# Performance work log

Hardware: AMD Instinct MI355X
Metric: run time of the kernel (lower is better)

Reference implementation:

```python
import jax, jax.numpy as jnp
import numpy as np

NEG = -1e30  # finite stand-in for -inf; exp underflows to 0 in fp32, grads stay finite


def setup_inputs() -> dict:
    key = jax.random.key(0)
    k1, k2, k3 = jax.random.split(key, 3)
    B, N, M = 64, 1024, 1024
    m = jax.random.normal(k1, (B, N, M), dtype=jnp.float32)
    nrows = jax.random.randint(k2, (B,), 0, N, dtype=jnp.int64) if jax.config.read('jax_enable_x64') else jax.random.randint(k2, (B,), 0, N, dtype=jnp.int32)
    ncols = jax.random.randint(k3, (B,), 0, M, dtype=jnp.int32)
    nrows = nrows.astype(jnp.int32)
    return {"m": m, "nrows": nrows, "ncols": ncols}


def reference(m, nrows, ncols):
    max_iter, tau = 20, 1.0
    B, N, M = m.shape  # N <= M -> no-transpose branch of the original
    row_valid = jnp.arange(N)[None, :, None] < nrows[:, None, None]  # [B,N,1]
    col_valid = jnp.arange(M)[None, None, :] < ncols[:, None, None]  # [B,1,M]
    valid = row_valid & col_valid                                    # [B,N,M]

    log_m = jnp.where(valid, m / tau, NEG)

    def step(lm, _):
        # even iteration: normalize rows (sum over columns)
        lse_r = jax.scipy.special.logsumexp(lm, axis=2, keepdims=True)  # [B,N,1]
        lm = jnp.where(valid, lm - lse_r, NEG)
        # odd iteration: normalize columns (sum over rows)
        lse_c = jax.scipy.special.logsumexp(lm, axis=1, keepdims=True)  # [B,1,M]
        lm = jnp.where(valid, lm - lse_c, NEG)
        return lm, None

    log_m, _ = jax.lax.scan(step, log_m, None, length=max_iter // 2)
    return jnp.where(valid, jnp.exp(log_m), 0.0)
```

## Files before the change

kernel.cpp:

```cpp
#include <hip/hip_runtime.h>
#include <math.h>


#define BIGNEG (-1e30f)
#define LOG2E 1.44269504f
typedef _Float16 h16;
struct alignas(16) h8 { h16 h[8]; };
typedef float f4 __attribute__((ext_vector_type(4)));

#define NN 1024
#define MM 1024
#define NBLK 16

__device__ __forceinline__ float wave_sum64(float v) {
#pragma unroll
    for (int o = 32; o > 0; o >>= 1) v += __shfl_xor(v, o, 64);
    return v;
}

__device__ __forceinline__ float ld_coh(const float* p) {
    return __hip_atomic_load(p, __ATOMIC_RELAXED, __HIP_MEMORY_SCOPE_AGENT);
}
__device__ __forceinline__ void st_coh(float* p, float v) {
    __hip_atomic_store(p, v, __ATOMIC_RELAXED, __HIP_MEMORY_SCOPE_AGENT);
}

__global__ void zero_bar(unsigned* bar, int n) {
    const int i = blockIdx.x * blockDim.x + threadIdx.x;
    if (i < n) bar[i] = 0;
}

#define BATCH_BAR()                                                            \
    do {                                                                       \
        asm volatile("s_waitcnt vmcnt(0)" ::: "memory");                       \
        __syncthreads();                                                       \
        ++phase;                                                               \
        if (threadIdx.x == 0) {                                                \
            __hip_atomic_fetch_add(ctr, 1u, __ATOMIC_RELAXED,                  \
                                   __HIP_MEMORY_SCOPE_AGENT);                  \
            while (__hip_atomic_load(ctr, __ATOMIC_RELAXED,                    \
                                     __HIP_MEMORY_SCOPE_AGENT) <               \
                   (unsigned)(phase * NBLK))                                   \
                __builtin_amdgcn_s_sleep(8);                                   \
        }                                                                      \
        __syncthreads();                                                       \
        asm volatile("" ::: "memory");                                         \
    } while (0)

__device__ __forceinline__ void sum16(const float* z, float* cs, float& u2) {
    float p[16], s = 0.f;
#pragma unroll
    for (int e = 0; e < 16; ++e) {
        p[e] = __builtin_amdgcn_exp2f(z[e]);
        s += p[e];
    }
    s = wave_sum64(s);
    const float rs = __builtin_amdgcn_rcpf(s);
#pragma unroll
    for (int e = 0; e < 16; ++e) cs[e] += p[e] * rs;
    u2 = -__builtin_amdgcn_logf(s);
}

__device__ __forceinline__ void nt_store4(float* p, f4 v) {
    __builtin_nontemporal_store(v, reinterpret_cast<f4*>(p));
}
__device__ __forceinline__ f4 nt_load4(const float* p) {
    return __builtin_nontemporal_load(reinterpret_cast<const f4*>(p));
}

__global__ __launch_bounds__(256, 4) void sinkhorn_fused(
    const float* __restrict__ m, const int* __restrict__ nrows,
    const int* __restrict__ ncols, float* __restrict__ P,
    h16* __restrict__ mh, unsigned* __restrict__ bar, float* __restrict__ out,
    int B) {
    const int sub = blockIdx.x & (NBLK - 1);
    const int b = blockIdx.x >> 4;
    const int w = threadIdx.x >> 6;
    const int lane = threadIdx.x & 63;
    const int wid = sub * 4 + w;
    const int tid = threadIdx.x;
    const int nr = nrows[b];
    const int nc = ncols[b];
    unsigned* ctr = bar + (size_t)b * 16;
    int phase = 0;

    __shared__ float pbuf[4][64][17];
    __shared__ float vloc[MM];
    __shared__ float uloc[NN];

    const size_t mbo = (size_t)b * NN * MM;
    const f4 z4 = {0.f, 0.f, 0.f, 0.f};

    if (nr == 0 || nc == 0) {
        for (int row = wid; row < NN; row += 64) {
            float* orow = out + mbo + (size_t)row * MM + lane * 8;
            nt_store4(orow, z4);
            nt_store4(orow + 4, z4);
            nt_store4(orow + 512, z4);
            nt_store4(orow + 516, z4);
        }
        return;
    }

    const size_t Psz = (size_t)B * NBLK * MM;
    float* Pw0 = P + (size_t)b * NBLK * MM + (size_t)sub * MM;
    const float* Pr0 = P + (size_t)b * NBLK * MM;

    float cs[16];
#pragma unroll
    for (int e = 0; e < 16; ++e) cs[e] = 0.f;

    {
        float mk[16];
#pragma unroll
        for (int e = 0; e < 16; ++e) {
            const int col = lane * 8 + (e >> 3) * 512 + (e & 7);
            mk[e] = (col < nc) ? 0.f : BIGNEG;
        }
        int row = wid;
        f4 A0, A1, A2, A3;
        if (row < nr) {
            const float* rp = m + mbo + (size_t)row * MM + lane * 8;
            A0 = nt_load4(rp);
            A1 = nt_load4(rp + 4);
            A2 = nt_load4(rp + 512);
            A3 = nt_load4(rp + 516);
        }
        while (row < nr) {
            const int nx = row + 64;
            f4 N0, N1, N2, N3;
            if (nx < nr) {
                const float* rq = m + mbo + (size_t)nx * MM + lane * 8;
                N0 = nt_load4(rq);
                N1 = nt_load4(rq + 4);
                N2 = nt_load4(rq + 512);
                N3 = nt_load4(rq + 516);
            }
            float zs[16], zr[16];
            *reinterpret_cast<f4*>(&zs[0]) = A0;
            *reinterpret_cast<f4*>(&zs[4]) = A1;
            *reinterpret_cast<f4*>(&zs[8]) = A2;
            *reinterpret_cast<f4*>(&zs[12]) = A3;
#pragma unroll
            for (int e = 0; e < 16; ++e) {
                zs[e] *= LOG2E;
                zr[e] = zs[e] + mk[e];
            }
            h8 hv0, hv1;
#pragma unroll
            for (int e = 0; e < 8; ++e) hv0.h[e] = (h16)zs[e];
#pragma unroll
            for (int e = 0; e < 8; ++e) hv1.h[e] = (h16)zs[8 + e];
            h16* rh = mh + mbo + (size_t)row * MM + lane * 8;
            *reinterpret_cast<h8*>(rh) = hv0;
            *reinterpret_cast<h8*>(rh + 512) = hv1;
            float u;
            sum16(zr, cs, u);
            if (lane == 0) uloc[row] = u;
            A0 = N0; A1 = N1; A2 = N2; A3 = N3;
            row = nx;
        }
    }

    for (int row = nr + wid; row < NN; row += 64) {
        float* orow = out + mbo + (size_t)row * MM + lane * 8;
        nt_store4(orow, z4);
        nt_store4(orow + 4, z4);
        nt_store4(orow + 512, z4);
        nt_store4(orow + 516, z4);
    }

    for (int t = 1; t <= 10; ++t) {
#pragma unroll
        for (int e = 0; e < 16; ++e) pbuf[w][lane][e] = cs[e];
        __syncthreads();
        {
            float* Pw = Pw0 + (size_t)(t & 1) * Psz;
#pragma unroll
            for (int q = 0; q < 4; ++q) {
                const int col = tid + q * 256;
                const int ls = (col >> 3) & 63;
                const int ei = ((col >> 9) << 3) | (col & 7);
                const float sum = pbuf[0][ls][ei] + pbuf[1][ls][ei] +
                                  pbuf[2][ls][ei] + pbuf[3][ls][ei];
                st_coh(Pw + col, sum);
            }
        }

        BATCH_BAR();

        {
            const float* Pr = Pr0 + (size_t)(t & 1) * Psz;
#pragma unroll
            for (int q = 0; q < 4; ++q) {
                const int col = tid + q * 256;
                float CS = 0.f;
#pragma unroll
                for (int s16 = 0; s16 < NBLK; ++s16)
                    CS += ld_coh(Pr + s16 * MM + col);
                const float vp = (t == 1) ? 0.f : vloc[col];
                const float vn = vp - __log2f(CS);
                vloc[col] = fminf(fmaxf(vn, BIGNEG), 1e30f);
            }
        }
        __syncthreads();
        if (t == 10) break;

        float vvm[16];
        {
            float tmp[16];
            *reinterpret_cast<f4*>(&tmp[0]) =
                *reinterpret_cast<const f4*>(&vloc[lane * 8]);
            *reinterpret_cast<f4*>(&tmp[4]) =
                *reinterpret_cast<const f4*>(&vloc[lane * 8 + 4]);
            *reinterpret_cast<f4*>(&tmp[8]) =
                *reinterpret_cast<const f4*>(&vloc[lane * 8 + 512]);
            *reinterpret_cast<f4*>(&tmp[12]) =
                *reinterpret_cast<const f4*>(&vloc[lane * 8 + 516]);
#pragma unroll
            for (int e = 0; e < 16; ++e) {
                const int col = lane * 8 + (e >> 3) * 512 + (e & 7);
                vvm[e] = (col < nc) ? tmp[e] : BIGNEG;
            }
        }
#pragma unroll
        for (int e = 0; e < 16; ++e) cs[e] = 0.f;
        {
            int row = wid;
            while (row + 64 < nr) {
                const h16* r0 = mh + mbo + (size_t)row * MM + lane * 8;
                const h16* r1 = r0 + (size_t)64 * MM;
                const h8 a0 = *reinterpret_cast<const h8*>(r0);
                const h8 a1 = *reinterpret_cast<const h8*>(r0 + 512);
                const h8 b0 = *reinterpret_cast<const h8*>(r1);
                const h8 b1 = *reinterpret_cast<const h8*>(r1 + 512);
                float z0[16], z1[16];
#pragma unroll
                for (int e = 0; e < 8; ++e) {
                    z0[e] = (float)a0.h[e] + vvm[e];
                    z0[8 + e] = (float)a1.h[e] + vvm[8 + e];
                    z1[e] = (float)b0.h[e] + vvm[e];
                    z1[8 + e] = (float)b1.h[e] + vvm[8 + e];
                }
                float u0, u1;
                sum16(z0, cs, u0);
                sum16(z1, cs, u1);
                if (lane == 0) { uloc[row] = u0; uloc[row + 64] = u1; }
                row += 128;
            }
            if (row < nr) {
                const h16* r0 = mh + mbo + (size_t)row * MM + lane * 8;
                const h8 a0 = *reinterpret_cast<const h8*>(r0);
                const h8 a1 = *reinterpret_cast<const h8*>(r0 + 512);
                float z0[16];
#pragma unroll
                for (int e = 0; e < 8; ++e) {
                    z0[e] = (float)a0.h[e] + vvm[e];
                    z0[8 + e] = (float)a1.h[e] + vvm[8 + e];
                }
                float u0;
                sum16(z0, cs, u0);
                if (lane == 0) uloc[row] = u0;
            }
        }
    }

    {
        float vvm[16];
        float tmp[16];
        *reinterpret_cast<f4*>(&tmp[0]) =
            *reinterpret_cast<const f4*>(&vloc[lane * 8]);
        *reinterpret_cast<f4*>(&tmp[4]) =
            *reinterpret_cast<const f4*>(&vloc[lane * 8 + 4]);
        *reinterpret_cast<f4*>(&tmp[8]) =
            *reinterpret_cast<const f4*>(&vloc[lane * 8 + 512]);
        *reinterpret_cast<f4*>(&tmp[12]) =
            *reinterpret_cast<const f4*>(&vloc[lane * 8 + 516]);
#pragma unroll
        for (int e = 0; e < 16; ++e) {
            const int col = lane * 8 + (e >> 3) * 512 + (e & 7);
            vvm[e] = (col < nc) ? tmp[e] : BIGNEG;
        }
        for (int row = wid; row < nr; row += 64) {
            float* orow = out + mbo + (size_t)row * MM + lane * 8;
            const float ui = uloc[row];
            const h16* rh = mh + mbo + (size_t)row * MM + lane * 8;
            const h8 h0 = *reinterpret_cast<const h8*>(rh);
            const h8 h1 = *reinterpret_cast<const h8*>(rh + 512);
            float r[16];
#pragma unroll
            for (int e = 0; e < 8; ++e) {
                r[e] = __builtin_amdgcn_exp2f((float)h0.h[e] + ui + vvm[e]);
                r[8 + e] =
                    __builtin_amdgcn_exp2f((float)h1.h[e] + ui + vvm[8 + e]);
            }
            nt_store4(orow, *reinterpret_cast<f4*>(&r[0]));
            nt_store4(orow + 4, *reinterpret_cast<f4*>(&r[4]));
            nt_store4(orow + 512, *reinterpret_cast<f4*>(&r[8]));
            nt_store4(orow + 516, *reinterpret_cast<f4*>(&r[12]));
        }
    }
}

extern "C" void kernel_launch(void* const* d_in, const int* in_sizes, int n_in,
                              void* d_out, int out_size, void* d_ws,
                              size_t ws_size, hipStream_t stream) {
    const float* m = (const float*)d_in[0];
    const int* nrows = (const int*)d_in[1];
    const int* ncols = (const int*)d_in[2];
    const int B = in_sizes[1];

    char* ws = (char*)d_ws;
    unsigned* bar = (unsigned*)ws;
    float* P = (float*)(ws + (1u << 20));
    h16* mh = (h16*)(ws + (16u << 20));
    float* out = (float*)d_out;

    const int nbar = B * 16;
    zero_bar<<<dim3((nbar + 255) / 256), dim3(256), 0, stream>>>(bar, nbar);

    sinkhorn_fused<<<dim3(B * NBLK), dim3(256), 0, stream>>>(
        m, nrows, ncols, P, mh, bar, out, B);
}
```

Measured before the change: 583.8 us.

## Pack column partial sums to fp16 and software-prefetch rows in sweep loops

Partial column sums exchanged between blocks through global memory are now packed as fp16 pairs in 32-bit words, halving the cross-block traffic at each barrier. The row-sweep and final output loops now prefetch the next rows' fp16 data into registers before computing on the current rows, to hide global load latency. Storing partial sums in fp16 loses precision and risks overflow in the sums; register pressure also increases.

Result: no change. 574.3 us (-1.6%).

```diff
diff --git a/kernel.cpp b/kernel.cpp
--- a/kernel.cpp
+++ b/kernel.cpp
@@ -18,10 +18,10 @@
     return v;
 }
 
-__device__ __forceinline__ float ld_coh(const float* p) {
+__device__ __forceinline__ unsigned ld_cohu(const unsigned* p) {
     return __hip_atomic_load(p, __ATOMIC_RELAXED, __HIP_MEMORY_SCOPE_AGENT);
 }
-__device__ __forceinline__ void st_coh(float* p, float v) {
+__device__ __forceinline__ void st_cohu(unsigned* p, unsigned v) {
     __hip_atomic_store(p, v, __ATOMIC_RELAXED, __HIP_MEMORY_SCOPE_AGENT);
 }
 
@@ -68,9 +68,20 @@
     return __builtin_nontemporal_load(reinterpret_cast<const f4*>(p));
 }
 
+__device__ __forceinline__ unsigned pack_h2(float a, float b) {
+    union { h16 h[2]; unsigned u; } r;
+    r.h[0] = (h16)a; r.h[1] = (h16)b;
+    return r.u;
+}
+__device__ __forceinline__ void unpack_h2(unsigned u, float& a, float& b) {
+    union { unsigned u; h16 h[2]; } r;
+    r.u = u;
+    a = (float)r.h[0]; b = (float)r.h[1];
+}
+
 __global__ __launch_bounds__(256, 4) void sinkhorn_fused(
     const float* __restrict__ m, const int* __restrict__ nrows,
-    const int* __restrict__ ncols, float* __restrict__ P,
+    const int* __restrict__ ncols, unsigned* __restrict__ P16,
     h16* __restrict__ mh, unsigned* __restrict__ bar, float* __restrict__ out,
     int B) {
     const int sub = blockIdx.x & (NBLK - 1);
@@ -102,9 +113,9 @@
         return;
     }
 
-    const size_t Psz = (size_t)B * NBLK * MM;
-    float* Pw0 = P + (size_t)b * NBLK * MM + (size_t)sub * MM;
-    const float* Pr0 = P + (size_t)b * NBLK * MM;
+    const size_t Psz = (size_t)B * NBLK * (MM / 2);
+    unsigned* Pw0 = P16 + ((size_t)b * NBLK + sub) * (MM / 2);
+    const unsigned* Pr0 = P16 + (size_t)b * NBLK * (MM / 2);
 
     float cs[16];
 #pragma unroll
@@ -175,32 +186,44 @@
         for (int e = 0; e < 16; ++e) pbuf[w][lane][e] = cs[e];
         __syncthreads();
         {
-            float* Pw = Pw0 + (size_t)(t & 1) * Psz;
-#pragma unroll
-            for (int q = 0; q < 4; ++q) {
-                const int col = tid + q * 256;
-                const int ls = (col >> 3) & 63;
-                const int ei = ((col >> 9) << 3) | (col & 7);
-                const float sum = pbuf[0][ls][ei] + pbuf[1][ls][ei] +
-                                  pbuf[2][ls][ei] + pbuf[3][ls][ei];
-                st_coh(Pw + col, sum);
+            unsigned* Pw = Pw0 + (size_t)(t & 1) * Psz;
+#pragma unroll
+            for (int q = 0; q < 2; ++q) {
+                const int pc = tid + q * 256;
+                float sm[2];
+#pragma unroll
+                for (int h = 0; h < 2; ++h) {
+                    const int col = 2 * pc + h;
+                    const int ls = (col >> 3) & 63;
+                    const int ei = ((col >> 9) << 3) | (col & 7);
+                    sm[h] = pbuf[0][ls][ei] + pbuf[1][ls][ei] +
+                            pbuf[2][ls][ei] + pbuf[3][ls][ei];
+                }
+                st_cohu(Pw + pc, pack_h2(sm[0], sm[1]));
             }
         }
 
         BATCH_BAR();
 
         {
-            const float* Pr = Pr0 + (size_t)(t & 1) * Psz;
-#pragma unroll
-            for (int q = 0; q < 4; ++q) {
-                const int col = tid + q * 256;
-                float CS = 0.f;
-#pragma unroll
-                for (int s16 = 0; s16 < NBLK; ++s16)
-                    CS += ld_coh(Pr + s16 * MM + col);
-                const float vp = (t == 1) ? 0.f : vloc[col];
-                const float vn = vp - __log2f(CS);
-                vloc[col] = fminf(fmaxf(vn, BIGNEG), 1e30f);
+            const unsigned* Pr = Pr0 + (size_t)(t & 1) * Psz;
+#pragma unroll
+            for (int q = 0; q < 2; ++q) {
+                const int pc = tid + q * 256;
+                float CS0 = 0.f, CS1 = 0.f;
+#pragma unroll
+                for (int s16 = 0; s16 < NBLK; ++s16) {
+                    float a, c;
+                    unpack_h2(ld_cohu(Pr + s16 * (MM / 2) + pc), a, c);
+                    CS0 += a; CS1 += c;
+                }
+                const int col = 2 * pc;
+                const float vp0 = (t == 1) ? 0.f : vloc[col];
+                const float vp1 = (t == 1) ? 0.f : vloc[col + 1];
+                const float vn0 = vp0 - __log2f(CS0);
+                const float vn1 = vp1 - __log2f(CS1);
+                vloc[col] = fminf(fmaxf(vn0, BIGNEG), 1e30f);
+                vloc[col + 1] = fminf(fmaxf(vn1, BIGNEG), 1e30f);
             }
         }
         __syncthreads();
@@ -227,40 +250,50 @@
         for (int e = 0; e < 16; ++e) cs[e] = 0.f;
         {
             int row = wid;
-            while (row + 64 < nr) {
-                const h16* r0 = mh + mbo + (size_t)row * MM + lane * 8;
-                const h16* r1 = r0 + (size_t)64 * MM;
-                const h8 a0 = *reinterpret_cast<const h8*>(r0);
-                const h8 a1 = *reinterpret_cast<const h8*>(r0 + 512);
-                const h8 b0 = *reinterpret_cast<const h8*>(r1);
-                const h8 b1 = *reinterpret_cast<const h8*>(r1 + 512);
-                float z0[16], z1[16];
+            h8 a0, a1, b0, b1;
+            if (row < nr) {
+                const int r2 = (row + 64 < nr) ? row + 64 : nr - 1;
+                const h16* p0 = mh + mbo + (size_t)row * MM + lane * 8;
+                const h16* p1 = mh + mbo + (size_t)r2 * MM + lane * 8;
+                a0 = *reinterpret_cast<const h8*>(p0);
+                a1 = *reinterpret_cast<const h8*>(p0 + 512);
+                b0 = *reinterpret_cast<const h8*>(p1);
+                b1 = *reinterpret_cast<const h8*>(p1 + 512);
+            }
+            while (row < nr) {
+                const int next = row + 128;
+                h8 na0, na1, nb0, nb1;
+                if (next < nr) {
+                    const int n2 = (next + 64 < nr) ? next + 64 : nr - 1;
+                    const h16* p0 = mh + mbo + (size_t)next * MM + lane * 8;
+                    const h16* p1 = mh + mbo + (size_t)n2 * MM + lane * 8;
+                    na0 = *reinterpret_cast<const h8*>(p0);
+                    na1 = *reinterpret_cast<const h8*>(p0 + 512);
+                    nb0 = *reinterpret_cast<const h8*>(p1);
+                    nb1 = *reinterpret_cast<const h8*>(p1 + 512);
+                }
+                float z0[16];
 #pragma unroll
                 for (int e = 0; e < 8; ++e) {
                     z0[e] = (float)a0.h[e] + vvm[e];
                     z0[8 + e] = (float)a1.h[e] + vvm[8 + e];
-                    z1[e] = (float)b0.h[e] + vvm[e];
-                    z1[8 + e] = (float)b1.h[e] + vvm[8 + e];
-                }
-                float u0, u1;
-                sum16(z0, cs, u0);
-                sum16(z1, cs, u1);
-                if (lane == 0) { uloc[row] = u0; uloc[row + 64] = u1; }
-                row += 128;
-            }
-            if (row < nr) {
-                const h16* r0 = mh + mbo + (size_t)row * MM + lane * 8;
-                const h8 a0 = *reinterpret_cast<const h8*>(r0);
-                const h8 a1 = *reinterpret_cast<const h8*>(r0 + 512);
-                float z0[16];
-#pragma unroll
-                for (int e = 0; e < 8; ++e) {
-                    z0[e] = (float)a0.h[e] + vvm[e];
-                    z0[8 + e] = (float)a1.h[e] + vvm[8 + e];
                 }
                 float u0;
                 sum16(z0, cs, u0);
                 if (lane == 0) uloc[row] = u0;
+                if (row + 64 < nr) {
+                    float z1[16];
+#pragma unroll
+                    for (int e = 0; e < 8; ++e) {
+                        z1[e] = (float)b0.h[e] + vvm[e];
+                        z1[8 + e] = (float)b1.h[e] + vvm[8 + e];
+                    }
+                    float u1;
+                    sum16(z1, cs, u1);
+                    if (lane == 0) uloc[row + 64] = u1;
+                }
+                a0 = na0; a1 = na1; b0 = nb0; b1 = nb1;
+                row = next;
             }
         }
     }
@@ -281,12 +314,23 @@
             const int col = lane * 8 + (e >> 3) * 512 + (e & 7);
             vvm[e] = (col < nc) ? tmp[e] : BIGNEG;
         }
-        for (int row = wid; row < nr; row += 64) {
+        int row = wid;
+        h8 h0, h1;
+        if (row < nr) {
+            const h16* rh = mh + mbo + (size_t)row * MM + lane * 8;
+            h0 = *reinterpret_cast<const h8*>(rh);
+            h1 = *reinterpret_cast<const h8*>(rh + 512);
+        }
+        while (row < nr) {
+            const int nx = row + 64;
+            h8 n0, n1;
+            if (nx < nr) {
+                const h16* rq = mh + mbo + (size_t)nx * MM + lane * 8;
+                n0 = *reinterpret_cast<const h8*>(rq);
+                n1 = *reinterpret_cast<const h8*>(rq + 512);
+            }
             float* orow = out + mbo + (size_t)row * MM + lane * 8;
             const float ui = uloc[row];
-            const h16* rh = mh + mbo + (size_t)row * MM + lane * 8;
-            const h8 h0 = *reinterpret_cast<const h8*>(rh);
-            const h8 h1 = *reinterpret_cast<const h8*>(rh + 512);
             float r[16];
 #pragma unroll
             for (int e = 0; e < 8; ++e) {
@@ -298,6 +342,8 @@
             nt_store4(orow + 4, *reinterpret_cast<f4*>(&r[4]));
             nt_store4(orow + 512, *reinterpret_cast<f4*>(&r[8]));
             nt_store4(orow + 516, *reinterpret_cast<f4*>(&r[12]));
+            h0 = n0; h1 = n1;
+            row = nx;
         }
     }
 }
@@ -312,7 +358,7 @@
 
     char* ws = (char*)d_ws;
     unsigned* bar = (unsigned*)ws;
-    float* P = (float*)(ws + (1u << 20));
+    unsigned* P16 = (unsigned*)(ws + (1u << 20));
     h16* mh = (h16*)(ws + (16u << 20));
     float* out = (float*)d_out;
 
@@ -320,5 +366,5 @@
     zero_bar<<<dim3((nbar + 255) / 256), dim3(256), 0, stream>>>(bar, nbar);
 
     sinkhorn_fused<<<dim3(B * NBLK), dim3(256), 0, stream>>>(
-        m, nrows, ncols, P, mh, bar, out, B);
-}
+        m, nrows, ncols, P16, mh, bar, out, B);
+}
```
